# Optimization experiments

Measured on AMD Instinct MI355X. Metric: run time of the kernel, lower is better.

The kernel has to match this reference:

```python
import jax, jax.numpy as jnp
import numpy as np

D_MODEL = 2048
N_HEADS = 16
N_KV_HEADS = 4
HEAD_DIM = D_MODEL // N_HEADS  # 128
ROPE_BASE = 10000.0


def _rope_tables(T, head_dim):
    half = head_dim // 2
    theta = 1.0 / (ROPE_BASE ** (jnp.arange(half, dtype=jnp.float32) / half))
    m = jnp.arange(T, dtype=jnp.float32)
    freqs = jnp.outer(m, theta)  # (T, half)
    return jnp.cos(freqs), jnp.sin(freqs)


def _apply_rope(x, cos, sin):
    # x: (B, H, T, hd); rotate first/second halves as pairs
    half = x.shape[-1] // 2
    x1, x2 = x[..., :half], x[..., half:]
    cos = cos[None, None, :, :]
    sin = sin[None, None, :, :]
    return jnp.concatenate([x1 * cos - x2 * sin, x1 * sin + x2 * cos], axis=-1)


def setup_inputs() -> dict:
    key = jax.random.key(0)
    ks = jax.random.split(key, 5)
    B, T = 4, 2048
    x = jax.random.normal(ks[0], (B, T, D_MODEL), dtype=jnp.float32)
    Wq = jax.random.normal(ks[1], (D_MODEL, N_HEADS * HEAD_DIM), dtype=jnp.float32) * 0.02
    Wk = jax.random.normal(ks[2], (D_MODEL, N_KV_HEADS * HEAD_DIM), dtype=jnp.float32) * 0.02
    Wv = jax.random.normal(ks[3], (D_MODEL, N_KV_HEADS * HEAD_DIM), dtype=jnp.float32) * 0.02
    Wo = jax.random.normal(ks[4], (N_HEADS * HEAD_DIM, D_MODEL), dtype=jnp.float32) * (0.02 / np.sqrt(2.0))
    return {"x": x, "Wq": Wq, "Wk": Wk, "Wv": Wv, "Wo": Wo}


def reference(x, Wq, Wk, Wv, Wo):
    B, T, C = x.shape
    groups = N_HEADS // N_KV_HEADS

    # QKV projections
    q = (x @ Wq).reshape(B, T, N_HEADS, HEAD_DIM).transpose(0, 2, 1, 3)      # (B,H,T,hd)
    k = (x @ Wk).reshape(B, T, N_KV_HEADS, HEAD_DIM).transpose(0, 2, 1, 3)   # (B,Hkv,T,hd)
    v = (x @ Wv).reshape(B, T, N_KV_HEADS, HEAD_DIM).transpose(0, 2, 1, 3)

    # RoPE on q and k
    cos, sin = _rope_tables(T, HEAD_DIM)
    q = _apply_rope(q, cos, sin)
    k = _apply_rope(k, cos, sin)

    # GQA: repeat each kv head `groups` times
    k = jnp.repeat(k, groups, axis=1)  # (B,H,T,hd)
    v = jnp.repeat(v, groups, axis=1)

    # Attention scores with ALiBi bias and causal mask
    scale = 1.0 / np.sqrt(HEAD_DIM)
    scores = jnp.einsum('bhqd,bhkd->bhqk', q, k) * scale  # (B,H,T,T)

    pos = jnp.arange(T)
    dist = jnp.minimum(pos[None, :] - pos[:, None], 0).astype(jnp.float32)  # (T,T), <=0
    slopes = 2.0 ** (-8.0 * jnp.arange(1, N_HEADS + 1, dtype=jnp.float32) / N_HEADS)
    alibi = slopes[:, None, None] * dist[None, :, :]  # (H,T,T)
    scores = scores + alibi[None]

    causal = pos[None, :] > pos[:, None]  # True = future = blocked
    scores = jnp.where(causal[None, None], -jnp.inf, scores)

    weights = jax.nn.softmax(scores, axis=-1)
    out = jnp.einsum('bhqk,bhkd->bhqd', weights, v)  # (B,H,T,hd)
    out = out.transpose(0, 2, 1, 3).reshape(B, T, N_HEADS * HEAD_DIM)
    return out @ Wo
```

## Files before the change

### kernel.cpp

```cpp
#include <hip/hip_runtime.h>
#include <hip/hip_bf16.h>
#include <stdint.h>

#define T_SEQ 2048
#define DM    2048
#define NH    16
#define NKVH  4
#define HD    128
#define NBATCH 4
#define BT    (NBATCH * T_SEQ)
#define ATT_SCALE 0.08838834764831845f
#define LOG2E 1.4426950408889634f

typedef __attribute__((ext_vector_type(8))) short bf16x8;
typedef __attribute__((ext_vector_type(4))) float f32x4;
typedef __attribute__((ext_vector_type(16))) float f32x16;
typedef __attribute__((ext_vector_type(8))) unsigned short ushort8;
typedef __attribute__((ext_vector_type(4))) unsigned short ushort4v;

static __device__ __forceinline__ unsigned short f2bf(float f) {
  __hip_bfloat16 h = __float2bfloat16(f);
  return __builtin_bit_cast(unsigned short, h);
}
static __device__ __forceinline__ float bf2f(unsigned short u) {
  unsigned int v = ((unsigned int)u) << 16;
  return __builtin_bit_cast(float, v);
}
static __device__ __forceinline__ unsigned int cvtpk(float a, float b) {
  unsigned int r;
  asm("v_cvt_pk_bf16_f32 %0, %1, %2" : "=v"(r) : "v"(a), "v"(b));
  return r;
}

#define GLDS16(g, l)                                                        \
  __builtin_amdgcn_global_load_lds(                                         \
      (const __attribute__((address_space(1))) void*)(g),                   \
      (__attribute__((address_space(3))) void*)(l), 16, 0, 0)

__global__ __launch_bounds__(256) void castx_k(const float* __restrict__ x,
                                               unsigned short* __restrict__ xb) {
  int i = (blockIdx.x * 256 + threadIdx.x) * 4;
  float4 v = *(const float4*)&x[i];
  ushort4v o;
  o[0] = f2bf(v.x); o[1] = f2bf(v.y); o[2] = f2bf(v.z); o[3] = f2bf(v.w);
  *(ushort4v*)&xb[i] = o;
}

__global__ __launch_bounds__(256) void transw_k(const float* __restrict__ src,
                                                unsigned short* __restrict__ dst,
                                                int ncols) {
  __shared__ unsigned short t[64][72];
  int n0 = blockIdx.x * 64, r0 = blockIdx.y * 64;
  int tid = threadIdx.x;
  int tx = tid & 15, ty = tid >> 4;
#pragma unroll
  for (int i = 0; i < 4; i++) {
    int r = ty * 4 + i;
    float4 v = *(const float4*)&src[(size_t)(r0 + r) * ncols + n0 + tx * 4];
    t[r][tx * 4 + 0] = f2bf(v.x);
    t[r][tx * 4 + 1] = f2bf(v.y);
    t[r][tx * 4 + 2] = f2bf(v.z);
    t[r][tx * 4 + 3] = f2bf(v.w);
  }
  __syncthreads();
  int nl = tid >> 2, seg = tid & 3;
  ushort8 o0, o1;
#pragma unroll
  for (int j = 0; j < 8; j++) {
    o0[j] = t[seg * 16 + j][nl];
    o1[j] = t[seg * 16 + 8 + j][nl];
  }
  size_t base = (size_t)(n0 + nl) * 2048 + r0 + seg * 16;
  *(ushort8*)&dst[base] = o0;
  *(ushort8*)&dst[base + 8] = o1;
}

template <int EPI>
__global__ __launch_bounds__(512) void gemm2_k(const unsigned short* __restrict__ A,
                                               const unsigned short* __restrict__ Bt,
                                               unsigned short* __restrict__ q_out,
                                               unsigned short* __restrict__ k_out,
                                               unsigned short* __restrict__ v_out,
                                               float* __restrict__ f_out) {
  __shared__ __align__(16) unsigned short smem[3 * 12288];

  const int tid = threadIdx.x;
  const int lane = tid & 63, wid = tid >> 6;
  const int wm = wid >> 2, wn = wid & 3;
  const int lr = lane & 15, lk = (lane >> 4) * 8;

  const int nwg = gridDim.x;
  const int cpx = nwg >> 3;
  const int swz = (blockIdx.x & 7) * cpx + (blockIdx.x >> 3);
  const int bx = swz & 63;
  const int by = swz >> 6;
  const int row0 = bx * 128, n00 = by * 256;

  const unsigned short* Aptr = A + (size_t)(row0 + (tid >> 2)) * 2048 + (tid & 3) * 8;
  const unsigned short* Bptr = Bt + (size_t)(n00 + (tid >> 2)) * 2048 + (tid & 3) * 8;

  f32x4 acc[4][4] = {};

#pragma unroll
  for (int p = 0; p < 2; p++) {
    unsigned short* s = &smem[p * 12288];
    GLDS16(Aptr + p * 32, &s[tid * 8]);
    GLDS16(Bptr + p * 32, &s[4096 + tid * 8]);
    GLDS16(Bptr + (size_t)128 * 2048 + p * 32, &s[8192 + tid * 8]);
  }

#pragma unroll 1
  for (int i = 0; i < 64; ++i) {
    if (i == 63) {
      asm volatile("s_waitcnt vmcnt(0)" ::: "memory");
    } else {
      asm volatile("s_waitcnt vmcnt(3)" ::: "memory");
    }
    asm volatile("s_barrier" ::: "memory");
    if (i + 2 < 64) {
      const int k0 = (i + 2) * 32;
      unsigned short* s = &smem[((i + 2) % 3) * 12288];
      GLDS16(Aptr + k0, &s[tid * 8]);
      GLDS16(Bptr + k0, &s[4096 + tid * 8]);
      GLDS16(Bptr + (size_t)128 * 2048 + k0, &s[8192 + tid * 8]);
    }

    const unsigned short* sA = &smem[(i % 3) * 12288];
    const unsigned short* sB = sA + 4096;
    bf16x8 af[4], bfr[4];
#pragma unroll
    for (int mi = 0; mi < 4; mi++)
      af[mi] = *(const bf16x8*)&sA[(wm * 64 + mi * 16 + lr) * 32 + lk];
#pragma unroll
    for (int ni = 0; ni < 4; ni++)
      bfr[ni] = *(const bf16x8*)&sB[(wn * 64 + ni * 16 + lr) * 32 + lk];

    __builtin_amdgcn_s_setprio(1);
#pragma unroll
    for (int mi = 0; mi < 4; mi++)
#pragma unroll
      for (int ni = 0; ni < 4; ni++)
        acc[mi][ni] =
            __builtin_amdgcn_mfma_f32_16x16x32_bf16(af[mi], bfr[ni], acc[mi][ni], 0, 0, 0);
    __builtin_amdgcn_s_setprio(0);
  }

  const int rbase = row0 + wm * 64;
  const int cbase = n00 + wn * 64;
#pragma unroll
  for (int mi = 0; mi < 4; mi++)
#pragma unroll
    for (int ni = 0; ni < 4; ni++)
#pragma unroll
      for (int r = 0; r < 4; r++) {
        int row = rbase + mi * 16 + (lane >> 4) * 4 + r;
        int col = cbase + ni * 16 + lr;
        float v = acc[mi][ni][r];
        if (EPI == 0) {
          if (col < 2048) {
            q_out[(size_t)row * 2048 + col] = f2bf(v);
          } else if (col < 2560) {
            k_out[(size_t)row * 512 + (col - 2048)] = f2bf(v);
          } else {
            int nv = col - 2560;
            int kvh = nv >> 7, d = nv & 127;
            int b = row >> 11, tt = row & 2047;
            v_out[((size_t)(b * NKVH + kvh) * HD + d) * T_SEQ + tt] = f2bf(v);
          }
        } else {
          f_out[(size_t)row * 2048 + col] = v;
        }
      }
}

__global__ __launch_bounds__(256) void rope_tab_k(float2* __restrict__ tab) {
  int idx = blockIdx.x * 256 + threadIdx.x;
  int t = idx >> 6, i = idx & 63;
  float theta = exp2f(-(float)i * (13.287712379549449f / 64.0f));
  float s, c;
  sincosf((float)t * theta, &s, &c);
  tab[idx] = make_float2(c, s);
}

__global__ __launch_bounds__(256) void rope_k(unsigned short* __restrict__ qb,
                                              unsigned short* __restrict__ kb,
                                              const float2* __restrict__ tab) {
  int idx = blockIdx.x * 256 + threadIdx.x;
  int i = idx & 63;
  int wi = idx >> 6;
  int hh = wi % (NH + NKVH);
  int bt = wi / (NH + NKVH);
  int t = bt & (T_SEQ - 1);
  unsigned short* p = (hh < NH) ? (qb + (size_t)bt * 2048 + hh * HD)
                                : (kb + (size_t)bt * 512 + (hh - NH) * HD);
  float2 cs = tab[(t << 6) + i];
  float x1 = bf2f(p[i]), x2 = bf2f(p[i + 64]);
  p[i] = f2bf(x1 * cs.x - x2 * cs.y);
  p[i + 64] = f2bf(x1 * cs.y + x2 * cs.x);
}

__global__ __launch_bounds__(256) void attn_k(const unsigned short* __restrict__ qb,
                                              const unsigned short* __restrict__ kb,
                                              const unsigned short* __restrict__ vt,
                                              unsigned short* __restrict__ ao) {
  __shared__ __align__(16) unsigned short smem[24576];

  const int bid = blockIdx.x;
  const int j = 15 - (bid >> 6);
  const int g = (bid & 7) | (((bid >> 3) & 1) << 3);
  const int hh = (bid >> 4) & 3;
  const int b = g >> 2, kvh = g & 3;
  const int h = kvh * 4 + hh;

  const int tid = threadIdx.x;
  const int wid = tid >> 6, lane = tid & 63;
  const int l31 = lane & 31, lh = lane >> 5;
  const int xr = l31 & 7;
  const float slope2 = exp2f(-0.5f * (float)(h + 1)) * LOG2E;
  const float scale2 = ATT_SCALE * LOG2E;

  const int q0 = j * 128 + wid * 32;
  const int dt_w = j * 4 + wid;
  const int nt = j * 4 + 4;

  const int krow = tid >> 4;
  const int cgk = (tid & 15) ^ (krow & 7);
  const int vr = tid >> 3;
  const int cgv = (tid & 7) ^ (vr & 7);

  const unsigned short* khead = kb + (size_t)(b * T_SEQ) * 512 + kvh * 128;
  const unsigned short* vhead = vt + (size_t)(b * NKVH + kvh) * HD * T_SEQ;

  auto stage = [&](int slot, int tile) {
    const int k0 = tile * 32;
    unsigned short* base = &smem[slot * 8192];
    GLDS16(khead + (size_t)(k0 + krow) * 512 + cgk * 8, base + tid * 8);
    GLDS16(khead + (size_t)(k0 + 16 + krow) * 512 + cgk * 8, base + 2048 + tid * 8);
    GLDS16(vhead + (size_t)(((cgv >> 2) << 6) + vr) * T_SEQ + k0 + (cgv & 3) * 8,
           base + 4096 + tid * 8);
    GLDS16(vhead + (size_t)(((cgv >> 2) << 6) + 32 + vr) * T_SEQ + k0 + (cgv & 3) * 8,
           base + 6144 + tid * 8);
  };

  unsigned short (*ot)[32][136] = (unsigned short(*)[32][136])smem;

  const unsigned short* qrow =
      qb + ((size_t)(b * T_SEQ + q0 + l31)) * 2048 + h * HD + lh * 8;
  bf16x8 qf[8];
#pragma unroll
  for (int ds = 0; ds < 8; ds++) qf[ds] = *(const bf16x8*)&qrow[ds * 16];

  f32x16 oacc[4] = {};
  float m2 = -1e30f, l_half = 0.f;
  const float arow = -slope2 * (float)(q0 + l31);

  float cr[16];
#pragma unroll
  for (int r = 0; r < 16; r++) {
    const int crow = (r & 3) + 8 * (r >> 2) + 4 * lh;
    cr[r] = fmaf(slope2, (float)crow, arow);
  }

  stage(0, nt - 1);
  stage(1, nt - 2);

#pragma unroll 1
  for (int it = 0; it < nt; ++it) {
    const int tt = nt - 1 - it;
    if (it == nt - 1) {
      asm volatile("s_waitcnt vmcnt(0)" ::: "memory");
    } else {
      asm volatile("s_waitcnt vmcnt(4)" ::: "memory");
    }
    asm volatile("s_barrier" ::: "memory");
    if (tt >= 2) stage((it + 2) % 3, tt - 2);

    if (tt <= dt_w) {
      const int slot = it % 3;
      const unsigned short* Kb = &smem[slot * 8192];
      const unsigned short* Vb = &smem[slot * 8192 + 4096];
      const int k0 = tt * 32;

      bf16x8 kf[8];
#pragma unroll
      for (int ds = 0; ds < 8; ds++)
        kf[ds] = *(const bf16x8*)&Kb[l31 * 128 + ((2 * ds + lh) ^ xr) * 8];

      __builtin_amdgcn_s_setprio(1);
      f32x16 sc = 0.f;
#pragma unroll
      for (int ds = 0; ds < 8; ds++)
        sc = __builtin_amdgcn_mfma_f32_32x32x16_bf16(kf[ds], qf[ds], sc, 0, 0, 0);
      __builtin_amdgcn_s_setprio(0);

      bf16x8 vf[4][2];
#pragma unroll
      for (int dt = 0; dt < 4; dt++)
#pragma unroll
        for (int ks = 0; ks < 2; ks++)
          vf[dt][ks] = *(const bf16x8*)&Vb[((dt & 1) * 32 + l31) * 64 +
                                           (((dt >> 1) * 4 + 2 * ks + lh) ^ xr) * 8];

      float s1[16];
#pragma unroll
      for (int r = 0; r < 16; r++) s1[r] = fmaf(sc[r], scale2, cr[r]);
      if (tt == dt_w) {
#pragma unroll
        for (int r = 0; r < 16; r++) {
          const int crow = (r & 3) + 8 * (r >> 2) + 4 * lh;
          if (crow > l31) s1[r] = -1e30f;
        }
      }

      float z = fmaf(slope2, (float)k0, -m2);

      float t8[8], t4[4];
#pragma unroll
      for (int i = 0; i < 8; i++) t8[i] = fmaxf(s1[i], s1[i + 8]);
#pragma unroll
      for (int i = 0; i < 4; i++) t4[i] = fmaxf(t8[i], t8[i + 4]);
      float mx = fmaxf(fmaxf(t4[0], t4[1]), fmaxf(t4[2], t4[3]));

      float pr[16];
#pragma unroll
      for (int r = 0; r < 16; r++) pr[r] = exp2f(s1[r] + z);

      mx = fmaxf(mx, __shfl_xor(mx, 32));
      if (__any(mx + z > 8.f)) {
        const float mt = (mx + z) + m2;
        const float mnew = fmaxf(m2, mt);
        const float corr = exp2f(m2 - mnew);
        l_half *= corr;
#pragma unroll
        for (int dt = 0; dt < 4; dt++) oacc[dt] *= corr;
        m2 = mnew;
        z = fmaf(slope2, (float)k0, -m2);
#pragma unroll
        for (int r = 0; r < 16; r++) pr[r] = exp2f(s1[r] + z);
      }

      float a8[8], a4[4];
#pragma unroll
      for (int i = 0; i < 8; i++) a8[i] = pr[i] + pr[i + 8];
#pragma unroll
      for (int i = 0; i < 4; i++) a4[i] = a8[i] + a8[i + 4];
      l_half += (a4[0] + a4[1]) + (a4[2] + a4[3]);

      unsigned int w[8];
#pragma unroll
      for (int i = 0; i < 8; i++) w[i] = cvtpk(pr[2 * i], pr[2 * i + 1]);
      const unsigned int ta = __shfl_xor(lh ? w[0] : w[2], 32);
      const unsigned int tb = __shfl_xor(lh ? w[1] : w[3], 32);
      const unsigned int tc = __shfl_xor(lh ? w[4] : w[6], 32);
      const unsigned int td = __shfl_xor(lh ? w[5] : w[7], 32);
      union U4 { unsigned int u[4]; bf16x8 v; } f0, f1;
      f0.u[0] = lh ? ta : w[0];
      f0.u[1] = lh ? tb : w[1];
      f0.u[2] = lh ? w[2] : ta;
      f0.u[3] = lh ? w[3] : tb;
      f1.u[0] = lh ? tc : w[4];
      f1.u[1] = lh ? td : w[5];
      f1.u[2] = lh ? w[6] : tc;
      f1.u[3] = lh ? w[7] : td;

      __builtin_amdgcn_s_setprio(1);
#pragma unroll
      for (int dt = 0; dt < 4; dt++) {
        oacc[dt] =
            __builtin_amdgcn_mfma_f32_32x32x16_bf16(vf[dt][0], f0.v, oacc[dt], 0, 0, 0);
        oacc[dt] =
            __builtin_amdgcn_mfma_f32_32x32x16_bf16(vf[dt][1], f1.v, oacc[dt], 0, 0, 0);
      }
      __builtin_amdgcn_s_setprio(0);
    }
  }

  const float l_tot = l_half + __shfl_xor(l_half, 32);
  const float inv = 1.0f / l_tot;
  __syncthreads();
#pragma unroll
  for (int dt = 0; dt < 4; dt++)
#pragma unroll
    for (int rg = 0; rg < 4; rg++) {
      ushort4v o;
#pragma unroll
      for (int jj = 0; jj < 4; jj++) o[jj] = f2bf(oacc[dt][rg * 4 + jj] * inv);
      *(ushort4v*)&ot[wid][l31][dt * 32 + rg * 8 + lh * 4] = o;
    }
  __syncthreads();
  const int rrow = lane >> 4, chunk = lane & 15;
#pragma unroll
  for (int ps = 0; ps < 8; ps++) {
    const int row = ps * 4 + rrow;
    ushort8 v = *(const ushort8*)&ot[wid][row][chunk * 8];
    *(ushort8*)&ao[((size_t)(b * T_SEQ + q0 + row)) * 2048 + h * HD + chunk * 8] = v;
  }
}

extern "C" void kernel_launch(void* const* d_in, const int* in_sizes, int n_in,
                              void* d_out, int out_size, void* d_ws, size_t ws_size,
                              hipStream_t stream) {
  const float* x = (const float*)d_in[0];
  const float* Wq = (const float*)d_in[1];
  const float* Wk = (const float*)d_in[2];
  const float* Wv = (const float*)d_in[3];
  const float* Wo = (const float*)d_in[4];

  char* w = (char*)d_ws;
  unsigned short* xb = (unsigned short*)w;
  unsigned short* wqt = (unsigned short*)(w + 33554432);
  unsigned short* qb = (unsigned short*)(w + 33554432 + 12582912);
  unsigned short* kb = (unsigned short*)(w + 33554432 + 12582912 + 33554432);
  unsigned short* vtb = (unsigned short*)(w + 33554432 + 12582912 + 33554432 + 8388608);
  float2* rtab = (float2*)w;

  castx_k<<<16384, 256, 0, stream>>>(x, xb);
  transw_k<<<dim3(32, 32), 256, 0, stream>>>(Wq, wqt, 2048);
  transw_k<<<dim3(8, 32), 256, 0, stream>>>(Wk, wqt + (size_t)2048 * 2048, 512);
  transw_k<<<dim3(8, 32), 256, 0, stream>>>(Wv, wqt + (size_t)2560 * 2048, 512);
  gemm2_k<0><<<768, 512, 0, stream>>>(xb, wqt, qb, kb, vtb, nullptr);
  rope_tab_k<<<512, 256, 0, stream>>>(rtab);
  rope_k<<<40960, 256, 0, stream>>>(qb, kb, rtab);
  transw_k<<<dim3(32, 32), 256, 0, stream>>>(Wo, wqt, 2048);
  attn_k<<<1024, 256, 0, stream>>>(qb, kb, vtb, xb);
  gemm2_k<1><<<512, 512, 0, stream>>>(xb, wqt, nullptr, nullptr, nullptr,
                                      (float*)d_out);
}
```

Before: 466.0 us.

## Enlarge GEMM tiles to 256x256 with BK=64, swizzled LDS and split-phase pipeline

```diff
diff --git a/kernel.cpp b/kernel.cpp
--- a/kernel.cpp
+++ b/kernel.cpp
@@ -76,84 +76,160 @@
 }
 
 template <int EPI>
-__global__ __launch_bounds__(512) void gemm2_k(const unsigned short* __restrict__ A,
+__global__ __launch_bounds__(512) void gemm8_k(const unsigned short* __restrict__ A,
                                                const unsigned short* __restrict__ Bt,
                                                unsigned short* __restrict__ q_out,
                                                unsigned short* __restrict__ k_out,
                                                unsigned short* __restrict__ v_out,
                                                float* __restrict__ f_out) {
-  __shared__ __align__(16) unsigned short smem[3 * 12288];
+  __shared__ __align__(16) unsigned short smem[65536];
 
   const int tid = threadIdx.x;
   const int lane = tid & 63, wid = tid >> 6;
   const int wm = wid >> 2, wn = wid & 3;
-  const int lr = lane & 15, lk = (lane >> 4) * 8;
+  const int lr = lane & 15, lq = lane >> 4;
+  const int sw = ((lr >> 2) & 1) << 1;
 
   const int nwg = gridDim.x;
   const int cpx = nwg >> 3;
   const int swz = (blockIdx.x & 7) * cpx + (blockIdx.x >> 3);
-  const int bx = swz & 63;
-  const int by = swz >> 6;
-  const int row0 = bx * 128, n00 = by * 256;
-
-  const unsigned short* Aptr = A + (size_t)(row0 + (tid >> 2)) * 2048 + (tid & 3) * 8;
-  const unsigned short* Bptr = Bt + (size_t)(n00 + (tid >> 2)) * 2048 + (tid & 3) * 8;
-
-  f32x4 acc[4][4] = {};
-
-#pragma unroll
-  for (int p = 0; p < 2; p++) {
-    unsigned short* s = &smem[p * 12288];
-    GLDS16(Aptr + p * 32, &s[tid * 8]);
-    GLDS16(Bptr + p * 32, &s[4096 + tid * 8]);
-    GLDS16(Bptr + (size_t)128 * 2048 + p * 32, &s[8192 + tid * 8]);
-  }
+  const int bx = swz & 31;
+  const int by = swz >> 5;
+  const int row0 = bx * 256, n00 = by * 256;
+
+  const int clog = (tid & 7) ^ (((tid >> 5) & 1) << 1);
+  const unsigned short* Asrc = A + (size_t)row0 * 2048 + clog * 8;
+  const unsigned short* Bsrc = Bt + (size_t)n00 * 2048 + clog * 8;
+
+  auto stageA = [&](int buf, int h, int k0) {
+#pragma unroll
+    for (int c = 0; c < 2; c++) {
+      const int rl = c * 128 + h * 64 + (tid >> 3);
+      GLDS16(Asrc + (size_t)rl * 2048 + k0,
+             &smem[buf * 32768 + (c * 128 + h * 64) * 64 + tid * 8]);
+    }
+  };
+  auto stageB = [&](int buf, int h, int k0) {
+#pragma unroll
+    for (int c = 0; c < 2; c++) {
+      const int pr = h * 128 + c * 64 + (tid >> 3);
+      const int p = pr >> 5;
+      const int l = (p < 4) ? (2 * p) : (2 * (p - 4) + 1);
+      const int logical = l * 32 + (pr & 31);
+      GLDS16(Bsrc + (size_t)logical * 2048 + k0,
+             &smem[buf * 32768 + 16384 + (h * 128 + c * 64) * 64 + tid * 8]);
+    }
+  };
+
+  auto ldA = [&](int buf, int rl, int kh) -> bf16x8 {
+    return *(const bf16x8*)&smem[buf * 32768 + rl * 64 + (((kh << 2) + lq) ^ sw) * 8];
+  };
+  auto ldB = [&](int buf, int ni, int kh) -> bf16x8 {
+    const int p = (ni < 2) ? wn : (4 + wn);
+    const int pr = p * 32 + (ni & 1) * 16 + lr;
+    return *(const bf16x8*)&smem[buf * 32768 + 16384 + pr * 64 +
+                                 (((kh << 2) + lq) ^ sw) * 8];
+  };
+
+  f32x4 acc[8][4] = {};
+
+  stageA(0, 0, 0);
+  stageB(0, 0, 0);
+  stageB(0, 1, 0);
+  stageA(0, 1, 0);
+
+  bf16x8 af[4][2], bfr[4][2];
 
 #pragma unroll 1
-  for (int i = 0; i < 64; ++i) {
-    if (i == 63) {
-      asm volatile("s_waitcnt vmcnt(0)" ::: "memory");
-    } else {
-      asm volatile("s_waitcnt vmcnt(3)" ::: "memory");
-    }
+  for (int t = 0; t < 32; ++t) {
+    const int buf = t & 1, obuf = buf ^ 1;
+    const bool nx = (t + 1 < 32);
+    const int k0n = (t + 1) << 6;
+
+    asm volatile("s_waitcnt vmcnt(4)" ::: "memory");
     asm volatile("s_barrier" ::: "memory");
-    if (i + 2 < 64) {
-      const int k0 = (i + 2) * 32;
-      unsigned short* s = &smem[((i + 2) % 3) * 12288];
-      GLDS16(Aptr + k0, &s[tid * 8]);
-      GLDS16(Bptr + k0, &s[4096 + tid * 8]);
-      GLDS16(Bptr + (size_t)128 * 2048 + k0, &s[8192 + tid * 8]);
-    }
-
-    const unsigned short* sA = &smem[(i % 3) * 12288];
-    const unsigned short* sB = sA + 4096;
-    bf16x8 af[4], bfr[4];
-#pragma unroll
-    for (int mi = 0; mi < 4; mi++)
-      af[mi] = *(const bf16x8*)&sA[(wm * 64 + mi * 16 + lr) * 32 + lk];
-#pragma unroll
-    for (int ni = 0; ni < 4; ni++)
-      bfr[ni] = *(const bf16x8*)&sB[(wn * 64 + ni * 16 + lr) * 32 + lk];
-
+#pragma unroll
+    for (int m = 0; m < 4; m++)
+#pragma unroll
+      for (int kh = 0; kh < 2; kh++) af[m][kh] = ldA(buf, wm * 128 + m * 16 + lr, kh);
+#pragma unroll
+    for (int ni = 0; ni < 2; ni++)
+#pragma unroll
+      for (int kh = 0; kh < 2; kh++) bfr[ni][kh] = ldB(buf, ni, kh);
+    if (nx) stageA(obuf, 0, k0n);
     __builtin_amdgcn_s_setprio(1);
 #pragma unroll
-    for (int mi = 0; mi < 4; mi++)
-#pragma unroll
-      for (int ni = 0; ni < 4; ni++)
-        acc[mi][ni] =
-            __builtin_amdgcn_mfma_f32_16x16x32_bf16(af[mi], bfr[ni], acc[mi][ni], 0, 0, 0);
+    for (int m = 0; m < 4; m++)
+#pragma unroll
+      for (int ni = 0; ni < 2; ni++)
+#pragma unroll
+        for (int kh = 0; kh < 2; kh++)
+          acc[m][ni] = __builtin_amdgcn_mfma_f32_16x16x32_bf16(af[m][kh], bfr[ni][kh],
+                                                               acc[m][ni], 0, 0, 0);
+    __builtin_amdgcn_s_setprio(0);
+
+    if (nx) asm volatile("s_waitcnt vmcnt(4)" ::: "memory");
+    else    asm volatile("s_waitcnt vmcnt(2)" ::: "memory");
+    asm volatile("s_barrier" ::: "memory");
+#pragma unroll
+    for (int ni = 2; ni < 4; ni++)
+#pragma unroll
+      for (int kh = 0; kh < 2; kh++) bfr[ni][kh] = ldB(buf, ni, kh);
+    if (nx) stageB(obuf, 0, k0n);
+    __builtin_amdgcn_s_setprio(1);
+#pragma unroll
+    for (int m = 0; m < 4; m++)
+#pragma unroll
+      for (int ni = 2; ni < 4; ni++)
+#pragma unroll
+        for (int kh = 0; kh < 2; kh++)
+          acc[m][ni] = __builtin_amdgcn_mfma_f32_16x16x32_bf16(af[m][kh], bfr[ni][kh],
+                                                               acc[m][ni], 0, 0, 0);
+    __builtin_amdgcn_s_setprio(0);
+
+    if (nx) asm volatile("s_waitcnt vmcnt(4)" ::: "memory");
+    else    asm volatile("s_waitcnt vmcnt(0)" ::: "memory");
+    asm volatile("s_barrier" ::: "memory");
+#pragma unroll
+    for (int m = 0; m < 4; m++)
+#pragma unroll
+      for (int kh = 0; kh < 2; kh++)
+        af[m][kh] = ldA(buf, wm * 128 + 64 + m * 16 + lr, kh);
+    if (nx) stageB(obuf, 1, k0n);
+    __builtin_amdgcn_s_setprio(1);
+#pragma unroll
+    for (int m = 0; m < 4; m++)
+#pragma unroll
+      for (int ni = 0; ni < 2; ni++)
+#pragma unroll
+        for (int kh = 0; kh < 2; kh++)
+          acc[4 + m][ni] = __builtin_amdgcn_mfma_f32_16x16x32_bf16(
+              af[m][kh], bfr[ni][kh], acc[4 + m][ni], 0, 0, 0);
+    __builtin_amdgcn_s_setprio(0);
+
+    asm volatile("s_barrier" ::: "memory");
+    if (nx) stageA(obuf, 1, k0n);
+    __builtin_amdgcn_s_setprio(1);
+#pragma unroll
+    for (int m = 0; m < 4; m++)
+#pragma unroll
+      for (int ni = 2; ni < 4; ni++)
+#pragma unroll
+        for (int kh = 0; kh < 2; kh++)
+          acc[4 + m][ni] = __builtin_amdgcn_mfma_f32_16x16x32_bf16(
+              af[m][kh], bfr[ni][kh], acc[4 + m][ni], 0, 0, 0);
     __builtin_amdgcn_s_setprio(0);
   }
 
-  const int rbase = row0 + wm * 64;
+  const int rbase = row0 + wm * 128;
   const int cbase = n00 + wn * 64;
 #pragma unroll
-  for (int mi = 0; mi < 4; mi++)
+  for (int mi = 0; mi < 8; mi++)
 #pragma unroll
     for (int ni = 0; ni < 4; ni++)
 #pragma unroll
       for (int r = 0; r < 4; r++) {
-        int row = rbase + mi * 16 + (lane >> 4) * 4 + r;
+        int row = rbase + mi * 16 + lq * 4 + r;
         int col = cbase + ni * 16 + lr;
         float v = acc[mi][ni][r];
         if (EPI == 0) {
@@ -418,11 +494,11 @@
   transw_k<<<dim3(32, 32), 256, 0, stream>>>(Wq, wqt, 2048);
   transw_k<<<dim3(8, 32), 256, 0, stream>>>(Wk, wqt + (size_t)2048 * 2048, 512);
   transw_k<<<dim3(8, 32), 256, 0, stream>>>(Wv, wqt + (size_t)2560 * 2048, 512);
-  gemm2_k<0><<<768, 512, 0, stream>>>(xb, wqt, qb, kb, vtb, nullptr);
+  gemm8_k<0><<<384, 512, 0, stream>>>(xb, wqt, qb, kb, vtb, nullptr);
   rope_tab_k<<<512, 256, 0, stream>>>(rtab);
   rope_k<<<40960, 256, 0, stream>>>(qb, kb, rtab);
   transw_k<<<dim3(32, 32), 256, 0, stream>>>(Wo, wqt, 2048);
   attn_k<<<1024, 256, 0, stream>>>(qb, kb, vtb, xb);
-  gemm2_k<1><<<512, 512, 0, stream>>>(xb, wqt, nullptr, nullptr, nullptr,
+  gemm8_k<1><<<256, 512, 0, stream>>>(xb, wqt, nullptr, nullptr, nullptr,
                                       (float*)d_out);
 }
```

New measurement: 474.0 us. Within noise of the previous version (+1.7%).
